# Optimization experiments

Measured on AMD Instinct MI355X. Metric: run time of the kernel, lower is better.

## Reference

```python
import jax, jax.numpy as jnp
import numpy as np

B, N_ELEC, N_NUC, D_EMB, D_MSG = 512, 32, 8, 128, 128


def idx_perm(n):
    # ordered pairs (i, j), i != j, shaped [n, n-1]
    i = np.repeat(np.arange(n), n - 1).reshape(n, n - 1)
    j = np.array([[k for k in range(n) if k != ii] for ii in range(n)])
    return jnp.asarray(i), jnp.asarray(j)


def pairwise_diffs(a, b):
    # a: [..., n, 3], b: [..., m, 3] -> [..., n, m, 4] (dx, dy, dz, |d|^2)
    d = a[..., :, None, :] - b[..., None, :, :]
    return jnp.concatenate([d, jnp.sum(d * d, axis=-1, keepdims=True)], axis=-1)


def mlp(x, w1, b1, w2, b2):
    return jax.nn.silu(x @ w1 + b1) @ w2 + b2


def setup_inputs() -> dict:
    key = jax.random.key(0)
    ks = jax.random.split(key, 10)
    sc = 0.1
    return {
        'rs': jax.random.normal(ks[0], (B, N_ELEC, 3), jnp.float32),
        'coords': jax.random.normal(ks[1], (N_NUC, 3), jnp.float32),
        'messages_el': jax.random.normal(ks[2], (B, N_ELEC, N_ELEC - 1, D_MSG), jnp.float32),
        'messages_nuc': jax.random.normal(ks[3], (B, N_ELEC, N_NUC, D_MSG), jnp.float32),
        'emb': jax.random.normal(ks[4], (B, N_ELEC, D_EMB), jnp.float32),
        'w1_el': jax.random.normal(ks[5], (D_EMB + D_MSG, 256), jnp.float32) * sc,
        'b1_el': jnp.zeros((256,), jnp.float32),
        'w2_el': jax.random.normal(ks[6], (256, 1), jnp.float32) * sc,
        'b2_el': jnp.zeros((1,), jnp.float32),
        'w1_nuc': jax.random.normal(ks[7], (D_EMB + D_MSG, 256), jnp.float32) * sc,
        'b1_nuc': jnp.zeros((256,), jnp.float32),
        'w2_nuc': jax.random.normal(ks[8], (256, 1), jnp.float32) * sc,
        'b2_nuc': jnp.zeros((1,), jnp.float32),
        'nuc_charges': jnp.array([6.0, 1.0, 1.0, 1.0, 1.0, 1.0, 1.0, 1.0], jnp.float32),
    }


def reference(rs, coords, messages_el, messages_nuc, emb,
              w1_el, b1_el, w2_el, b2_el,
              w1_nuc, b1_nuc, w2_nuc, b2_nuc, nuc_charges):
    n_elec, n_nuc = rs.shape[-2], coords.shape[0]
    emb_p = emb[:, :, None]  # [B, n_elec, 1, D_emb]
    # gather-concat features per pair
    f_el = jnp.concatenate(
        [jnp.broadcast_to(emb_p, (B, n_elec, n_elec - 1, D_EMB)), messages_el], axis=-1)
    f_nuc = jnp.concatenate(
        [jnp.broadcast_to(emb_p, (B, n_elec, n_nuc, D_EMB)), messages_nuc], axis=-1)
    i, j = idx_perm(n_elec)
    diffs_nuc = pairwise_diffs(rs, coords)  # [B, n_elec, n_nuc, 4]
    diffs_ee = pairwise_diffs(-rs, -rs)[:, i, j]  # [B, n_elec, n_elec-1, 4]
    diffs = jnp.concatenate([diffs_ee, diffs_nuc], axis=-2)
    f = jnp.concatenate(
        [mlp(f_el, w1_el, b1_el, w2_el, b2_el),
         mlp(f_nuc, w1_nuc, b1_nuc, w2_nuc, b2_nuc)], axis=-2)  # [B, n_elec, P, 1]
    ps = f * diffs[..., :3] / (1.0 + diffs[..., 3:] ** 1.5)
    ps = ps.sum(axis=-2)  # [B, n_elec, 3]
    # deeperwin decay
    decay = jnp.tanh(diffs_nuc[..., -1] / (0.5 / nuc_charges) ** 2).prod(axis=-1)
    return np.exp(-3.5).astype(np.float32) * decay[..., None] * ps
```

## Files before the change

kernel.cpp:

```cpp
#include <hip/hip_runtime.h>
#include <hip/hip_bf16.h>

#define OUT_SCALE 0.030197383422318501f

typedef __attribute__((ext_vector_type(8))) short bf16x8;
typedef __attribute__((ext_vector_type(4))) float f32x4;

#define EL_BLOCKS 2048
#define NUC_BLOCKS 1024

__device__ __forceinline__ unsigned pk2(float a, float b) {
  __hip_bfloat162 h = __float22bfloat162_rn(make_float2(a, b));
  unsigned u;
  __builtin_memcpy(&u, &h, 4);
  return u;
}

__device__ __forceinline__ float silu_f(float h) {
  return h * __builtin_amdgcn_rcpf(1.0f + __expf(-h));
}

__global__ void prep_w1(const float* __restrict__ w1a,
                        const float* __restrict__ w1b,
                        unsigned short* __restrict__ wp) {
  int gid = blockIdx.x * 256 + threadIdx.x;
  const float* w1 = (gid < 8192) ? w1a : w1b;
  int rem = gid & 8191;
  int kk = rem >> 10;
  int kg = (rem >> 8) & 3;
  int col = rem & 255;
  const float* src = w1 + (kk * 32 + kg * 8) * 256 + col;
  uint4 v;
  v.x = pk2(src[0 * 256], src[1 * 256]);
  v.y = pk2(src[2 * 256], src[3 * 256]);
  v.z = pk2(src[4 * 256], src[5 * 256]);
  v.w = pk2(src[6 * 256], src[7 * 256]);
  *(uint4*)(wp + (size_t)gid * 8) = v;
}

__global__ __launch_bounds__(512, 4) void bf_main_kernel(
    const float* __restrict__ rs, const float* __restrict__ msg_el,
    const float* __restrict__ msg_nuc, const float* __restrict__ emb,
    const unsigned short* __restrict__ wpk,
    const float* __restrict__ b1_el, const float* __restrict__ w2_el,
    const float* __restrict__ b2_el,
    const float* __restrict__ b1_nuc, const float* __restrict__ w2_nuc,
    const float* __restrict__ b2_nuc,
    const float* __restrict__ coords, const float* __restrict__ chg,
    float* __restrict__ out) {
  __shared__ __align__(16) unsigned short s_emb[16 * 128];
  __shared__ __align__(16) unsigned short s_msg[256 * 128];
  __shared__ float s_fp[8][256];
  __shared__ float s_ps[16][4];
  __shared__ float s_decay[16];

  const int tid = threadIdx.x;
  const int bid = blockIdx.x;
  const int lane = tid & 63;
  const int wv = tid >> 6;
  const int cIdx = lane & 15, kg = lane >> 4;

  if (bid < EL_BLOCKS) {
    const int gp0 = bid * 8;
    const float* msg = msg_el;

    if (tid < 32) ((float*)s_ps)[tid] = 0.0f;

    if (tid < 128) {
      int p = tid >> 4, c = tid & 15;
      const float* src = emb + (gp0 + p) * 128 + c * 8;
      float4 v0 = *(const float4*)src;
      float4 v1 = *(const float4*)(src + 4);
      uint4 pk;
      pk.x = pk2(v0.x, v0.y); pk.y = pk2(v0.z, v0.w);
      pk.z = pk2(v1.x, v1.y); pk.w = pk2(v1.z, v1.w);
      *(uint4*)(s_emb + p * 128 + c * 8) = pk;
    }

#pragma unroll
    for (int it = 0; it < 8; ++it) {
      int id = it * 512 + tid;
      int r = id >> 4, c = id & 15;
      int p = r >> 5, j = r & 31;
      uint4 pk = {0u, 0u, 0u, 0u};
      if (j < 31) {
        const float* src = msg + (size_t)((gp0 + p) * 31 + j) * 128 + c * 8;
        float4 v0 = *(const float4*)src;
        float4 v1 = *(const float4*)(src + 4);
        pk.x = pk2(v0.x, v0.y); pk.y = pk2(v0.z, v0.w);
        pk.z = pk2(v1.x, v1.y); pk.w = pk2(v1.z, v1.w);
      }
      int sw = c ^ (r & 15);
      *(uint4*)(s_msg + r * 128 + sw * 8) = pk;
    }

    bf16x8 Bf[8][2];
    float b1v[2][4], w2v[2][4];
#pragma unroll
    for (int nt = 0; nt < 2; ++nt) {
#pragma unroll
      for (int reg = 0; reg < 4; ++reg) {
        int h = wv * 32 + nt * 16 + kg * 4 + reg;
        b1v[nt][reg] = b1_el[h];
        w2v[nt][reg] = w2_el[h];
      }
      int col = wv * 32 + nt * 16 + cIdx;
#pragma unroll
      for (int kk = 0; kk < 8; ++kk)
        Bf[kk][nt] = *(const bf16x8*)(wpk + (size_t)((kk * 4 + kg) * 256 + col) * 8);
    }

    __syncthreads();

#pragma unroll 1
    for (int t = 0; t < 16; ++t) {
      int p = t >> 1;
      int r = t * 16 + cIdx;
      int rx = r & 15;
      const unsigned short* ep = s_emb + p * 128 + kg * 8;
      const unsigned short* mp = s_msg + r * 128;
      f32x4 acc0 = {b1v[0][0], b1v[0][1], b1v[0][2], b1v[0][3]};
      f32x4 acc1 = {b1v[1][0], b1v[1][1], b1v[1][2], b1v[1][3]};
#pragma unroll
      for (int kk = 0; kk < 8; ++kk) {
        bf16x8 a;
        if (kk < 4) {
          a = *(const bf16x8*)(ep + kk * 32);
        } else {
          int sw = (((kk - 4) * 4 + kg) ^ rx);
          a = *(const bf16x8*)(mp + sw * 8);
        }
        acc0 = __builtin_amdgcn_mfma_f32_16x16x32_bf16(Bf[kk][0], a, acc0, 0, 0, 0);
        acc1 = __builtin_amdgcn_mfma_f32_16x16x32_bf16(Bf[kk][1], a, acc1, 0, 0, 0);
      }
      float p0 = 0.0f, p1 = 0.0f;
#pragma unroll
      for (int reg = 0; reg < 4; ++reg) {
        p0 += silu_f(acc0[reg]) * w2v[0][reg];
        p1 += silu_f(acc1[reg]) * w2v[1][reg];
      }
      float v = p0 + p1;
      v += __shfl_xor(v, 16);
      v += __shfl_xor(v, 32);
      if (kg == 0) s_fp[wv][t * 16 + cIdx] = v;
    }

    __syncthreads();

    if (tid < 248) {
      int p = tid / 31, jj = tid - p * 31;
      int gp = gp0 + p, b = gp >> 5, i = gp & 31;
      int jidx = jj + (jj >= i ? 1 : 0);
      const float* rsb = rs + b * 96;
      float dx = rsb[jidx * 3 + 0] - rsb[i * 3 + 0];
      float dy = rsb[jidx * 3 + 1] - rsb[i * 3 + 1];
      float dz = rsb[jidx * 3 + 2] - rsb[i * 3 + 2];
      float tq = dx * dx + dy * dy + dz * dz;
      int row = p * 32 + jj;
      float f = b2_el[0];
#pragma unroll
      for (int w = 0; w < 8; ++w) f += s_fp[w][row];
      float g = f * __builtin_amdgcn_rcpf(1.0f + tq * sqrtf(tq));
      atomicAdd(&s_ps[p][0], g * dx);
      atomicAdd(&s_ps[p][1], g * dy);
      atomicAdd(&s_ps[p][2], g * dz);
    }
    if (tid < 8) {
      int gp = gp0 + tid, b = gp >> 5, i = gp & 31;
      float x = rs[(b * 32 + i) * 3 + 0];
      float y = rs[(b * 32 + i) * 3 + 1];
      float z = rs[(b * 32 + i) * 3 + 2];
      float dcy = 1.0f;
#pragma unroll
      for (int n = 0; n < 8; ++n) {
        float dx = x - coords[n * 3 + 0];
        float dy = y - coords[n * 3 + 1];
        float dz = z - coords[n * 3 + 2];
        float tq = dx * dx + dy * dy + dz * dz;
        float zc = chg[n];
        dcy *= tanhf(4.0f * tq * zc * zc);
      }
      s_decay[tid] = dcy;
    }
    __syncthreads();
    if (tid < 24) {
      int p = tid / 3, c = tid - p * 3;
      int gp = gp0 + p;
      atomicAdd(&out[gp * 3 + c], OUT_SCALE * s_decay[p] * s_ps[p][c]);
    }
  } else {
    const int nbid = bid - EL_BLOCKS;
    const int gp0 = nbid * 16;
    const float* msg = msg_nuc;
    const unsigned short* wp = wpk + 8192 * 8;

    if (tid < 64) ((float*)s_ps)[tid] = 0.0f;

    if (tid < 256) {
      int p = tid >> 4, c = tid & 15;
      const float* src = emb + (gp0 + p) * 128 + c * 8;
      float4 v0 = *(const float4*)src;
      float4 v1 = *(const float4*)(src + 4);
      uint4 pk;
      pk.x = pk2(v0.x, v0.y); pk.y = pk2(v0.z, v0.w);
      pk.z = pk2(v1.x, v1.y); pk.w = pk2(v1.z, v1.w);
      *(uint4*)(s_emb + p * 128 + c * 8) = pk;
    }

#pragma unroll
    for (int it = 0; it < 4; ++it) {
      int id = it * 512 + tid;
      int r = id >> 4, c = id & 15;
      const float* src = msg + (size_t)(gp0 * 8 + r) * 128 + c * 8;
      float4 v0 = *(const float4*)src;
      float4 v1 = *(const float4*)(src + 4);
      uint4 pk;
      pk.x = pk2(v0.x, v0.y); pk.y = pk2(v0.z, v0.w);
      pk.z = pk2(v1.x, v1.y); pk.w = pk2(v1.z, v1.w);
      int sw = c ^ (r & 15);
      *(uint4*)(s_msg + r * 128 + sw * 8) = pk;
    }

    bf16x8 Bf[8][2];
    float b1v[2][4], w2v[2][4];
#pragma unroll
    for (int nt = 0; nt < 2; ++nt) {
#pragma unroll
      for (int reg = 0; reg < 4; ++reg) {
        int h = wv * 32 + nt * 16 + kg * 4 + reg;
        b1v[nt][reg] = b1_nuc[h];
        w2v[nt][reg] = w2_nuc[h];
      }
      int col = wv * 32 + nt * 16 + cIdx;
#pragma unroll
      for (int kk = 0; kk < 8; ++kk)
        Bf[kk][nt] = *(const bf16x8*)(wp + (size_t)((kk * 4 + kg) * 256 + col) * 8);
    }

    __syncthreads();

#pragma unroll 1
    for (int t = 0; t < 8; ++t) {
      int r = t * 16 + cIdx;
      int p = r >> 3;
      int rx = r & 15;
      const unsigned short* ep = s_emb + p * 128 + kg * 8;
      const unsigned short* mp = s_msg + r * 128;
      f32x4 acc0 = {b1v[0][0], b1v[0][1], b1v[0][2], b1v[0][3]};
      f32x4 acc1 = {b1v[1][0], b1v[1][1], b1v[1][2], b1v[1][3]};
#pragma unroll
      for (int kk = 0; kk < 8; ++kk) {
        bf16x8 a;
        if (kk < 4) {
          a = *(const bf16x8*)(ep + kk * 32);
        } else {
          int sw = (((kk - 4) * 4 + kg) ^ rx);
          a = *(const bf16x8*)(mp + sw * 8);
        }
        acc0 = __builtin_amdgcn_mfma_f32_16x16x32_bf16(Bf[kk][0], a, acc0, 0, 0, 0);
        acc1 = __builtin_amdgcn_mfma_f32_16x16x32_bf16(Bf[kk][1], a, acc1, 0, 0, 0);
      }
      float p0 = 0.0f, p1 = 0.0f;
#pragma unroll
      for (int reg = 0; reg < 4; ++reg) {
        p0 += silu_f(acc0[reg]) * w2v[0][reg];
        p1 += silu_f(acc1[reg]) * w2v[1][reg];
      }
      float v = p0 + p1;
      v += __shfl_xor(v, 16);
      v += __shfl_xor(v, 32);
      if (kg == 0) s_fp[wv][t * 16 + cIdx] = v;
    }

    __syncthreads();

    if (tid < 128) {
      int p = tid >> 3, n = tid & 7;
      int gp = gp0 + p, b = gp >> 5, i = gp & 31;
      float dx = rs[(b * 32 + i) * 3 + 0] - coords[n * 3 + 0];
      float dy = rs[(b * 32 + i) * 3 + 1] - coords[n * 3 + 1];
      float dz = rs[(b * 32 + i) * 3 + 2] - coords[n * 3 + 2];
      float tq = dx * dx + dy * dy + dz * dz;
      float f = b2_nuc[0];
#pragma unroll
      for (int w = 0; w < 8; ++w) f += s_fp[w][tid];
      float g = f * __builtin_amdgcn_rcpf(1.0f + tq * sqrtf(tq));
      atomicAdd(&s_ps[p][0], g * dx);
      atomicAdd(&s_ps[p][1], g * dy);
      atomicAdd(&s_ps[p][2], g * dz);
    }
    if (tid < 16) {
      int gp = gp0 + tid, b = gp >> 5, i = gp & 31;
      float x = rs[(b * 32 + i) * 3 + 0];
      float y = rs[(b * 32 + i) * 3 + 1];
      float z = rs[(b * 32 + i) * 3 + 2];
      float dcy = 1.0f;
#pragma unroll
      for (int n = 0; n < 8; ++n) {
        float dx = x - coords[n * 3 + 0];
        float dy = y - coords[n * 3 + 1];
        float dz = z - coords[n * 3 + 2];
        float tq = dx * dx + dy * dy + dz * dz;
        float zc = chg[n];
        dcy *= tanhf(4.0f * tq * zc * zc);
      }
      s_decay[tid] = dcy;
    }
    __syncthreads();
    if (tid < 48) {
      int p = tid / 3, c = tid - p * 3;
      int gp = gp0 + p;
      atomicAdd(&out[gp * 3 + c], OUT_SCALE * s_decay[p] * s_ps[p][c]);
    }
  }
}

extern "C" void kernel_launch(void* const* d_in, const int* in_sizes, int n_in,
                              void* d_out, int out_size, void* d_ws, size_t ws_size,
                              hipStream_t stream) {
  const float* rs       = (const float*)d_in[0];
  const float* coords   = (const float*)d_in[1];
  const float* msg_el   = (const float*)d_in[2];
  const float* msg_nuc  = (const float*)d_in[3];
  const float* emb      = (const float*)d_in[4];
  const float* w1_el    = (const float*)d_in[5];
  const float* b1_el    = (const float*)d_in[6];
  const float* w2_el    = (const float*)d_in[7];
  const float* b2_el    = (const float*)d_in[8];
  const float* w1_nuc   = (const float*)d_in[9];
  const float* b1_nuc   = (const float*)d_in[10];
  const float* w2_nuc   = (const float*)d_in[11];
  const float* b2_nuc   = (const float*)d_in[12];
  const float* chg      = (const float*)d_in[13];
  float* out = (float*)d_out;

  unsigned short* wpk = (unsigned short*)d_ws;

  hipMemsetAsync(out, 0, (size_t)out_size * sizeof(float), stream);
  prep_w1<<<64, 256, 0, stream>>>(w1_el, w1_nuc, wpk);
  bf_main_kernel<<<EL_BLOCKS + NUC_BLOCKS, 512, 0, stream>>>(
      rs, msg_el, msg_nuc, emb, wpk, b1_el, w2_el, b2_el, b1_nuc, w2_nuc,
      b2_nuc, coords, chg, out);
}
```

Before: 132.9 us.

## Load message rows directly from global into MFMA operands, dropping LDS staging

Removes the shared-memory staging buffer for message features in both the electron and nucleus paths. Each wave now reads its message rows from global memory inside the MFMA loop and converts them to bf16 in registers; padding rows are masked to zero. The goal is to free 64KB of LDS per block, which could allow more resident blocks, and to cut the LDS write/read round trip. The cost is that all 8 waves, which split the hidden columns, each reload and re-convert the same rows, so L1/L2 traffic rises about 8x. Load latency is also exposed per iteration because the loop is not unrolled.

```diff
diff --git a/kernel.cpp b/kernel.cpp
--- a/kernel.cpp
+++ b/kernel.cpp
@@ -14,6 +14,17 @@
   unsigned u;
   __builtin_memcpy(&u, &h, 4);
   return u;
+}
+
+__device__ __forceinline__ bf16x8 pack8(float4 lo, float4 hi, bool valid) {
+  uint4 u;
+  u.x = valid ? pk2(lo.x, lo.y) : 0u;
+  u.y = valid ? pk2(lo.z, lo.w) : 0u;
+  u.z = valid ? pk2(hi.x, hi.y) : 0u;
+  u.w = valid ? pk2(hi.z, hi.w) : 0u;
+  bf16x8 a;
+  __builtin_memcpy(&a, &u, 16);
+  return a;
 }
 
 __device__ __forceinline__ float silu_f(float h) {
@@ -49,7 +60,6 @@
     const float* __restrict__ coords, const float* __restrict__ chg,
     float* __restrict__ out) {
   __shared__ __align__(16) unsigned short s_emb[16 * 128];
-  __shared__ __align__(16) unsigned short s_msg[256 * 128];
   __shared__ float s_fp[8][256];
   __shared__ float s_ps[16][4];
   __shared__ float s_decay[16];
@@ -77,23 +87,6 @@
       *(uint4*)(s_emb + p * 128 + c * 8) = pk;
     }
 
-#pragma unroll
-    for (int it = 0; it < 8; ++it) {
-      int id = it * 512 + tid;
-      int r = id >> 4, c = id & 15;
-      int p = r >> 5, j = r & 31;
-      uint4 pk = {0u, 0u, 0u, 0u};
-      if (j < 31) {
-        const float* src = msg + (size_t)((gp0 + p) * 31 + j) * 128 + c * 8;
-        float4 v0 = *(const float4*)src;
-        float4 v1 = *(const float4*)(src + 4);
-        pk.x = pk2(v0.x, v0.y); pk.y = pk2(v0.z, v0.w);
-        pk.z = pk2(v1.x, v1.y); pk.w = pk2(v1.z, v1.w);
-      }
-      int sw = c ^ (r & 15);
-      *(uint4*)(s_msg + r * 128 + sw * 8) = pk;
-    }
-
     bf16x8 Bf[8][2];
     float b1v[2][4], w2v[2][4];
 #pragma unroll
@@ -116,22 +109,31 @@
     for (int t = 0; t < 16; ++t) {
       int p = t >> 1;
       int r = t * 16 + cIdx;
-      int rx = r & 15;
+      int j = r & 31;
+      bool valid = j < 31;
+      int jc = valid ? j : 30;
+      const float* mrow =
+          msg + ((size_t)((gp0 + p) * 31 + jc)) * 128 + kg * 8;
+      float4 m0[4], m1[4];
+#pragma unroll
+      for (int kk = 0; kk < 4; ++kk) {
+        m0[kk] = *(const float4*)(mrow + kk * 32);
+        m1[kk] = *(const float4*)(mrow + kk * 32 + 4);
+      }
       const unsigned short* ep = s_emb + p * 128 + kg * 8;
-      const unsigned short* mp = s_msg + r * 128;
       f32x4 acc0 = {b1v[0][0], b1v[0][1], b1v[0][2], b1v[0][3]};
       f32x4 acc1 = {b1v[1][0], b1v[1][1], b1v[1][2], b1v[1][3]};
 #pragma unroll
-      for (int kk = 0; kk < 8; ++kk) {
-        bf16x8 a;
-        if (kk < 4) {
-          a = *(const bf16x8*)(ep + kk * 32);
-        } else {
-          int sw = (((kk - 4) * 4 + kg) ^ rx);
-          a = *(const bf16x8*)(mp + sw * 8);
-        }
+      for (int kk = 0; kk < 4; ++kk) {
+        bf16x8 a = *(const bf16x8*)(ep + kk * 32);
         acc0 = __builtin_amdgcn_mfma_f32_16x16x32_bf16(Bf[kk][0], a, acc0, 0, 0, 0);
         acc1 = __builtin_amdgcn_mfma_f32_16x16x32_bf16(Bf[kk][1], a, acc1, 0, 0, 0);
+      }
+#pragma unroll
+      for (int kk = 0; kk < 4; ++kk) {
+        bf16x8 a = pack8(m0[kk], m1[kk], valid);
+        acc0 = __builtin_amdgcn_mfma_f32_16x16x32_bf16(Bf[kk + 4][0], a, acc0, 0, 0, 0);
+        acc1 = __builtin_amdgcn_mfma_f32_16x16x32_bf16(Bf[kk + 4][1], a, acc1, 0, 0, 0);
       }
       float p0 = 0.0f, p1 = 0.0f;
 #pragma unroll
@@ -207,20 +209,6 @@
       *(uint4*)(s_emb + p * 128 + c * 8) = pk;
     }
 
-#pragma unroll
-    for (int it = 0; it < 4; ++it) {
-      int id = it * 512 + tid;
-      int r = id >> 4, c = id & 15;
-      const float* src = msg + (size_t)(gp0 * 8 + r) * 128 + c * 8;
-      float4 v0 = *(const float4*)src;
-      float4 v1 = *(const float4*)(src + 4);
-      uint4 pk;
-      pk.x = pk2(v0.x, v0.y); pk.y = pk2(v0.z, v0.w);
-      pk.z = pk2(v1.x, v1.y); pk.w = pk2(v1.z, v1.w);
-      int sw = c ^ (r & 15);
-      *(uint4*)(s_msg + r * 128 + sw * 8) = pk;
-    }
-
     bf16x8 Bf[8][2];
     float b1v[2][4], w2v[2][4];
 #pragma unroll
@@ -243,22 +231,27 @@
     for (int t = 0; t < 8; ++t) {
       int r = t * 16 + cIdx;
       int p = r >> 3;
-      int rx = r & 15;
+      const float* mrow = msg + ((size_t)(gp0 * 8 + r)) * 128 + kg * 8;
+      float4 m0[4], m1[4];
+#pragma unroll
+      for (int kk = 0; kk < 4; ++kk) {
+        m0[kk] = *(const float4*)(mrow + kk * 32);
+        m1[kk] = *(const float4*)(mrow + kk * 32 + 4);
+      }
       const unsigned short* ep = s_emb + p * 128 + kg * 8;
-      const unsigned short* mp = s_msg + r * 128;
       f32x4 acc0 = {b1v[0][0], b1v[0][1], b1v[0][2], b1v[0][3]};
       f32x4 acc1 = {b1v[1][0], b1v[1][1], b1v[1][2], b1v[1][3]};
 #pragma unroll
-      for (int kk = 0; kk < 8; ++kk) {
-        bf16x8 a;
-        if (kk < 4) {
-          a = *(const bf16x8*)(ep + kk * 32);
-        } else {
-          int sw = (((kk - 4) * 4 + kg) ^ rx);
-          a = *(const bf16x8*)(mp + sw * 8);
-        }
+      for (int kk = 0; kk < 4; ++kk) {
+        bf16x8 a = *(const bf16x8*)(ep + kk * 32);
         acc0 = __builtin_amdgcn_mfma_f32_16x16x32_bf16(Bf[kk][0], a, acc0, 0, 0, 0);
         acc1 = __builtin_amdgcn_mfma_f32_16x16x32_bf16(Bf[kk][1], a, acc1, 0, 0, 0);
+      }
+#pragma unroll
+      for (int kk = 0; kk < 4; ++kk) {
+        bf16x8 a = pack8(m0[kk], m1[kk], true);
+        acc0 = __builtin_amdgcn_mfma_f32_16x16x32_bf16(Bf[kk + 4][0], a, acc0, 0, 0, 0);
+        acc1 = __builtin_amdgcn_mfma_f32_16x16x32_bf16(Bf[kk + 4][1], a, acc1, 0, 0, 0);
       }
       float p0 = 0.0f, p1 = 0.0f;
 #pragma unroll
```

After: 391.3 us. +194.5%, slower.
